# Kernel optimization log

Measured on AMD Instinct MI355X. Metric: run time of the kernel, lower is better.

Reference implementation:

```python
import jax, jax.numpy as jnp
import numpy as np

B, H, W = 1, 48, 160
CIN, CF, D = 1024, 64, 48  # input_features, PSM_features, depth_channel = max_disp/downsample
EPS = 1e-5


def setup_inputs() -> dict:
    key = jax.random.key(0)
    ks = jax.random.split(key, 12)
    z = lambda s: jnp.zeros(s, jnp.float32)
    o = lambda s: jnp.ones(s, jnp.float32)
    return {
        "left_features": jax.random.normal(ks[0], (B, CIN, H, W), jnp.float32),
        "right_features": jax.random.normal(ks[1], (B, CIN, H, W), jnp.float32),
        "conv1_w": jax.random.normal(ks[2], (CF, CIN), jnp.float32) * 0.03,
        "conv1_b": z((CF,)),
        "bn1_g": o((CF,)), "bn1_b": z((CF,)),
        "bn1_m": jax.random.normal(ks[3], (CF,), jnp.float32) * 0.1,
        "bn1_v": jax.random.uniform(ks[4], (CF,), jnp.float32) + 0.5,
        "c3a_w": jax.random.normal(ks[5], (CF, 2 * CF, 3, 3, 3), jnp.float32) * 0.02,
        "c3a_b": z((CF,)),
        "bn3a_g": o((CF,)), "bn3a_b": z((CF,)),
        "bn3a_m": jax.random.normal(ks[6], (CF,), jnp.float32) * 0.1,
        "bn3a_v": jax.random.uniform(ks[7], (CF,), jnp.float32) + 0.5,
        "c3b_w": jax.random.normal(ks[8], (CF, CF, 3, 3, 3), jnp.float32) * 0.02,
        "c3b_b": z((CF,)),
        "bn3b_g": o((CF,)), "bn3b_b": z((CF,)),
        "bn3b_m": jax.random.normal(ks[9], (CF,), jnp.float32) * 0.1,
        "bn3b_v": jax.random.uniform(ks[10], (CF,), jnp.float32) + 0.5,
    }


def _bn(x, g, b, m, v, nsp):
    # eval-mode batchnorm; nsp = number of trailing spatial dims
    sh = (-1,) + (1,) * nsp
    return (x - m.reshape(sh)) * (g.reshape(sh) * jax.lax.rsqrt(v.reshape(sh) + EPS)) + b.reshape(sh)


def reference(left_features, right_features, conv1_w, conv1_b, bn1_g, bn1_b, bn1_m, bn1_v,
              c3a_w, c3a_b, bn3a_g, bn3a_b, bn3a_m, bn3a_v,
              c3b_w, c3b_b, bn3b_g, bn3b_b, bn3b_m, bn3b_v):
    def down(x):
        y = jnp.einsum('oi,bihw->bohw', conv1_w, x) + conv1_b[:, None, None]
        return jax.nn.relu(_bn(y, bn1_g, bn1_b, bn1_m, bn1_v, 2))

    L = down(left_features)   # [B,CF,H,W]
    R = down(right_features)  # [B,CF,H,W]

    # Vectorized shifted cost volume (replaces the Python loop over disparities).
    # For disparity d, output width j: left -> L[...,j] if j>=d else 0; right -> R[...,j-d] if j>=d else 0.
    idx = jnp.arange(W)[None, :] - jnp.arange(D)[:, None]       # [D,W]
    mask = (idx >= 0).astype(L.dtype)                           # [D,W]
    left_vol = L[:, :, :, None, :] * mask                       # [B,CF,H,D,W]
    right_vol = R[:, :, :, jnp.clip(idx, 0, W - 1)] * mask      # [B,CF,H,D,W]
    cost = jnp.concatenate([left_vol, right_vol], axis=1)       # [B,2CF,H,D,W]
    cost = jnp.transpose(cost, (0, 1, 3, 2, 4))                 # [B,2CF,D,H,W]

    def conv3(x, wk, bias):
        y = jax.lax.conv_general_dilated(x, wk, (1, 1, 1), [(1, 1)] * 3,
                                         dimension_numbers=('NCDHW', 'OIDHW', 'NCDHW'))
        return y + bias[:, None, None, None]

    y = jax.nn.relu(_bn(conv3(cost, c3a_w, c3a_b), bn3a_g, bn3a_b, bn3a_m, bn3a_v, 3))
    y = jax.nn.relu(_bn(conv3(y, c3b_w, c3b_b), bn3b_g, bn3b_b, bn3b_m, bn3b_v, 3))
    return y.reshape(B, -1, H, W)  # [B, CF*D, H, W]
```

## Files before the change

kernel.cpp:

```cpp
#include <hip/hip_runtime.h>
#include <hip/hip_bf16.h>


#define HH   48
#define WW   160
#define DDEP 48
#define CIN  1024
#define NPX  (HH*WW)
#define KSPL 8

typedef unsigned short u16;
typedef unsigned int   u32;
typedef __attribute__((ext_vector_type(8))) short bf16x8;
typedef __attribute__((ext_vector_type(4))) float f32x4;
typedef __attribute__((ext_vector_type(4))) u32   u32x4;
typedef __attribute__((ext_vector_type(2))) u32   u32x2;

__device__ __forceinline__ u16 f2bf(float f) {
    u32 u = __builtin_bit_cast(u32, f);
    u32 r = u + 0x7FFFu + ((u >> 16) & 1u);
    return (u16)(r >> 16);
}

__global__ __launch_bounds__(256) void k_prep(
    const float* __restrict__ c3a, const float* __restrict__ c3b,
    const float* __restrict__ cb3a, const float* __restrict__ g3a,
    const float* __restrict__ b3a,  const float* __restrict__ m3a,
    const float* __restrict__ v3a,
    const float* __restrict__ cb3b, const float* __restrict__ g3b,
    const float* __restrict__ b3b,  const float* __restrict__ m3b,
    const float* __restrict__ v3b,
    u16* __restrict__ wa, u16* __restrict__ wb, float* __restrict__ bnc)
{
    int tid = blockIdx.x*256 + threadIdx.x;
    if (tid < 221184) {
        int i = tid & 127, o = (tid >> 7) & 63, tap = tid >> 13;
        wa[tid] = f2bf(c3a[(o*128 + i)*27 + tap]);
    } else {
        int t2 = tid - 221184;
        if (t2 < 110592) {
            int i = t2 & 63;
            int kw = (t2 >> 6) % 3;
            int rest = t2 / 192;
            int o = rest & 63, kdkh = rest >> 6;
            wb[t2] = f2bf(c3b[(o*64 + i)*27 + (kdkh/3)*9 + (kdkh%3)*3 + kw]);
        }
    }
    if (tid < 64) {
        float s = g3a[tid] * rsqrtf(v3a[tid] + 1e-5f);
        bnc[tid]      = s;
        bnc[64 + tid] = (cb3a[tid] - m3a[tid])*s + b3a[tid];
    } else if (tid < 128) {
        int o = tid - 64;
        float s = g3b[o] * rsqrtf(v3b[o] + 1e-5f);
        bnc[128 + o] = s;
        bnc[192 + o] = (cb3b[o] - m3b[o])*s + b3b[o];
    }
}

__global__ __launch_bounds__(256) void k_conv1(
    const float* __restrict__ left, const float* __restrict__ right,
    const float* __restrict__ w1, float* __restrict__ P)
{
    const int img = blockIdx.y;
    const int s   = blockIdx.z;
    const float* x = img ? right : left;
    const int px = blockIdx.x*64 + (threadIdx.x & 63);
    const int o0 = (threadIdx.x >> 6)*16;

    float acc[16];
    #pragma unroll
    for (int oo = 0; oo < 16; ++oo) acc[oo] = 0.f;

    const int ibase = s*(CIN/KSPL);
    for (int it = 0; it < CIN/KSPL; it += 4) {
        const int i = ibase + it;
        float x0 = x[(i+0)*NPX + px];
        float x1 = x[(i+1)*NPX + px];
        float x2 = x[(i+2)*NPX + px];
        float x3 = x[(i+3)*NPX + px];
        #pragma unroll
        for (int oo = 0; oo < 16; ++oo) {
            const float4 wv4 = *(const float4*)(w1 + (size_t)(o0+oo)*CIN + i);
            acc[oo] = fmaf(wv4.w, x3, fmaf(wv4.z, x2,
                      fmaf(wv4.y, x1, fmaf(wv4.x, x0, acc[oo]))));
        }
    }
    float* dst = P + ((size_t)(s*2 + img)*NPX + px)*64 + o0;
    #pragma unroll
    for (int q = 0; q < 4; ++q)
        *(f32x4*)(dst + q*4) = *(const f32x4*)(acc + q*4);
}

__global__ __launch_bounds__(256) void k_conv1_reduce(
    const float* __restrict__ P,
    const float* __restrict__ b1,
    const float* __restrict__ g,  const float* __restrict__ bb,
    const float* __restrict__ m,  const float* __restrict__ v,
    u16* __restrict__ LRb)
{
    const int tid = blockIdx.x*256 + threadIdx.x;
    const int f = tid*4;
    f32x4 acc = *(const f32x4*)(P + f);
    #pragma unroll
    for (int s = 1; s < KSPL; ++s)
        acc += *(const f32x4*)(P + (size_t)(s*2)*(NPX*64) + f);
    const int o0 = f & 63;
    u16 res[4];
    #pragma unroll
    for (int r = 0; r < 4; ++r) {
        int o = o0 + r;
        float sc = g[o] * rsqrtf(v[o] + 1e-5f);
        float val = (acc[r] + b1[o] - m[o])*sc + bb[o];
        res[r] = f2bf(val > 0.f ? val : 0.f);
    }
    *(u32x2*)(LRb + f) = *(const u32x2*)res;
}

__global__ __launch_bounds__(256) void k_conv3a(
    const u16* __restrict__ LRb, const u16* __restrict__ wa,
    const float* __restrict__ bnc, u16* __restrict__ yt)
{
    __shared__ u16 sm[31744];
    u16* Lt = sm;
    u16* Rt = sm + 11520;
    u16* Aw = sm + 23040;

    const int h  = blockIdx.x;
    const int d0 = blockIdx.y*2;
    const int tid = threadIdx.x;
    const int l  = tid & 63;
    const int wv = tid >> 6;
    const int dd = wv >> 1;
    const int wbase = (wv & 1)*80;
    const int l15 = l & 15, l4 = l >> 4;
    const int wcol = wbase + l15;
    const bf16x8 bzero = {0,0,0,0,0,0,0,0};

    f32x4 acc[4][5];
    #pragma unroll
    for (int a = 0; a < 4; ++a)
        #pragma unroll
        for (int b = 0; b < 5; ++b)
            acc[a][b] = (f32x4){0.f,0.f,0.f,0.f};

    for (int kh = 0; kh < 3; ++kh) {
        int hp = h + kh - 1;
        if (hp < 0 || hp >= HH) continue;
        __syncthreads();
        {
            const u16* ls = LRb + (size_t)hp*WW*64;
            const u16* rs = LRb + (size_t)NPX*64 + (size_t)hp*WW*64;
            #pragma unroll
            for (int gq = 0; gq < 5; ++gq) {
                int eb = (gq*256 + tid)*8;
                int wwi = eb >> 6, ii = eb & 63;
                u32x4 va = *(const u32x4*)(ls + eb);
                u32x4 vb = *(const u32x4*)(rs + eb);
                *(u32x4*)(Lt + wwi*72 + ii) = va;
                *(u32x4*)(Rt + wwi*72 + ii) = vb;
            }
        }
        for (int kd = 0; kd < 3; ++kd) {
            int dp = d0 + dd + kd - 1;
            bool dok = (dp >= 0) && (dp < DDEP);
            for (int kw = 0; kw < 3; ++kw) {
                __syncthreads();
                {
                    const u16* as = wa + (size_t)(kd*9 + kh*3 + kw)*8192;
                    #pragma unroll
                    for (int gq = 0; gq < 4; ++gq) {
                        int eb = (gq*256 + tid)*8;
                        int o = eb >> 7, ii = eb & 127;
                        *(u32x4*)(Aw + o*136 + ii) = *(const u32x4*)(as + eb);
                    }
                }
                __syncthreads();

                int laddr[5], raddr[5];
                bool val[5];
                #pragma unroll
                for (int nf = 0; nf < 5; ++nf) {
                    int wp = wcol + nf*16 + kw - 1;
                    bool vv = dok && (wp >= 0) && (wp < WW) && (wp >= dp);
                    val[nf]   = vv;
                    laddr[nf] = (vv ? wp : 0)*72;
                    raddr[nf] = (vv ? (wp - dp) : 0)*72;
                }
                #pragma unroll
                for (int ic = 0; ic < 4; ++ic) {
                    const int kcolA = ic*32 + 8*l4;
                    bf16x8 a0 = *(const bf16x8*)(Aw + ( 0 + l15)*136 + kcolA);
                    bf16x8 a1 = *(const bf16x8*)(Aw + (16 + l15)*136 + kcolA);
                    bf16x8 a2 = *(const bf16x8*)(Aw + (32 + l15)*136 + kcolA);
                    bf16x8 a3 = *(const bf16x8*)(Aw + (48 + l15)*136 + kcolA);
                    const int kin = (ic & 1)*32 + 8*l4;
                    #pragma unroll
                    for (int nf = 0; nf < 5; ++nf) {
                        const u16* bp = (ic < 2) ? (Lt + laddr[nf] + kin)
                                                 : (Rt + raddr[nf] + kin);
                        bf16x8 b = *(const bf16x8*)bp;
                        b = val[nf] ? b : bzero;
                        acc[0][nf] = __builtin_amdgcn_mfma_f32_16x16x32_bf16(a0, b, acc[0][nf], 0, 0, 0);
                        acc[1][nf] = __builtin_amdgcn_mfma_f32_16x16x32_bf16(a1, b, acc[1][nf], 0, 0, 0);
                        acc[2][nf] = __builtin_amdgcn_mfma_f32_16x16x32_bf16(a2, b, acc[2][nf], 0, 0, 0);
                        acc[3][nf] = __builtin_amdgcn_mfma_f32_16x16x32_bf16(a3, b, acc[3][nf], 0, 0, 0);
                    }
                }
            }
        }
    }

    __syncthreads();
    u16* eps = sm + wv*5280;
    float sc[4][4], sh[4][4];
    #pragma unroll
    for (int mf = 0; mf < 4; ++mf)
        #pragma unroll
        for (int r = 0; r < 4; ++r) {
            int o = mf*16 + 4*l4 + r;
            sc[mf][r] = bnc[o];
            sh[mf][r] = bnc[64 + o];
        }
    #pragma unroll
    for (int mf = 0; mf < 4; ++mf)
        #pragma unroll
        for (int nf = 0; nf < 5; ++nf)
            #pragma unroll
            for (int r = 0; r < 4; ++r) {
                float vv = acc[mf][nf][r]*sc[mf][r] + sh[mf][r];
                vv = vv > 0.f ? vv : 0.f;
                eps[(nf*16 + l15)*66 + mf*16 + 4*l4 + r] = f2bf(vv);
            }
    const size_t rowbase = (size_t)((d0 + dd)*HH + h)*WW + wbase;
    u16* yb = yt + rowbase*64;
    #pragma unroll
    for (int k = 0; k < 40; ++k) {
        int flat = k*64 + l;
        int n = flat >> 5, odw = (flat & 31)*2;
        u32 vv = *(const u32*)(eps + n*66 + odw);
        *(u32*)(yb + (size_t)n*64 + odw) = vv;
    }
}

__global__ __launch_bounds__(256) void k_conv3b(
    const u16* __restrict__ yt, const u16* __restrict__ wb,
    const float* __restrict__ bnc, float* __restrict__ outp)
{
    __shared__ u16 sm2[35840];
    u16* Bt0 = sm2;
    u16* Bt1 = sm2 + 11520;
    u16* A2  = sm2 + 23040;

    const int h  = blockIdx.x;
    const int d0 = blockIdx.y*2;
    const int tid = threadIdx.x;
    const int l  = tid & 63;
    const int wv = tid >> 6;
    const int dd = wv >> 1;
    const int wbase = (wv & 1)*80;
    const int l15 = l & 15, l4 = l >> 4;
    const int wcol = wbase + l15;
    const bf16x8 bzero = {0,0,0,0,0,0,0,0};

    f32x4 acc[4][5];
    #pragma unroll
    for (int a = 0; a < 4; ++a)
        #pragma unroll
        for (int b = 0; b < 5; ++b)
            acc[a][b] = (f32x4){0.f,0.f,0.f,0.f};

    for (int kh = 0; kh < 3; ++kh) {
        int hp = h + kh - 1;
        if (hp < 0 || hp >= HH) continue;
        for (int kd = 0; kd < 3; ++kd) {
            __syncthreads();
            {
                int dpa = d0 + kd - 1, dpb = d0 + kd;
                int ca = min(max(dpa, 0), DDEP-1);
                int cb = min(max(dpb, 0), DDEP-1);
                const u16* s0 = yt + ((size_t)(ca*HH + hp)*WW)*64;
                const u16* s1 = yt + ((size_t)(cb*HH + hp)*WW)*64;
                #pragma unroll
                for (int gq = 0; gq < 5; ++gq) {
                    int eb = (gq*256 + tid)*8;
                    int wwi = eb >> 6, ii = eb & 63;
                    *(u32x4*)(Bt0 + wwi*72 + ii) = *(const u32x4*)(s0 + eb);
                    *(u32x4*)(Bt1 + wwi*72 + ii) = *(const u32x4*)(s1 + eb);
                }
                const u16* as = wb + (size_t)(kd*3 + kh)*12288;
                #pragma unroll
                for (int gq = 0; gq < 6; ++gq) {
                    int idx = gq*256 + tid;
                    int o = idx/24;
                    int c = (idx - o*24)*8;
                    *(u32x4*)(A2 + o*200 + c) = *(const u32x4*)(as + (size_t)idx*8);
                }
            }
            __syncthreads();

            int dpw = d0 + dd + kd - 1;
            bool dok = (dpw >= 0) && (dpw < DDEP);
            const u16* Bt = dd ? Bt1 : Bt0;
            for (int kw = 0; kw < 3; ++kw) {
                int baddr[5]; bool val[5];
                #pragma unroll
                for (int nf = 0; nf < 5; ++nf) {
                    int wp = wcol + nf*16 + kw - 1;
                    bool vv = dok && (wp >= 0) && (wp < WW);
                    val[nf]   = vv;
                    baddr[nf] = (vv ? wp : 0)*72;
                }
                #pragma unroll
                for (int ic = 0; ic < 2; ++ic) {
                    const int kcolA = kw*64 + ic*32 + 8*l4;
                    bf16x8 a0 = *(const bf16x8*)(A2 + ( 0 + l15)*200 + kcolA);
                    bf16x8 a1 = *(const bf16x8*)(A2 + (16 + l15)*200 + kcolA);
                    bf16x8 a2 = *(const bf16x8*)(A2 + (32 + l15)*200 + kcolA);
                    bf16x8 a3 = *(const bf16x8*)(A2 + (48 + l15)*200 + kcolA);
                    const int kin = ic*32 + 8*l4;
                    #pragma unroll
                    for (int nf = 0; nf < 5; ++nf) {
                        bf16x8 b = *(const bf16x8*)(Bt + baddr[nf] + kin);
                        b = val[nf] ? b : bzero;
                        acc[0][nf] = __builtin_amdgcn_mfma_f32_16x16x32_bf16(a0, b, acc[0][nf], 0, 0, 0);
                        acc[1][nf] = __builtin_amdgcn_mfma_f32_16x16x32_bf16(a1, b, acc[1][nf], 0, 0, 0);
                        acc[2][nf] = __builtin_amdgcn_mfma_f32_16x16x32_bf16(a2, b, acc[2][nf], 0, 0, 0);
                        acc[3][nf] = __builtin_amdgcn_mfma_f32_16x16x32_bf16(a3, b, acc[3][nf], 0, 0, 0);
                    }
                }
            }
        }
    }

    const int dout = d0 + dd;
    #pragma unroll
    for (int mf = 0; mf < 4; ++mf)
        #pragma unroll
        for (int r = 0; r < 4; ++r) {
            int o = mf*16 + 4*l4 + r;
            float s = bnc[128 + o], t = bnc[192 + o];
            size_t base = ((size_t)(o*DDEP + dout)*HH + h)*WW + wbase;
            #pragma unroll
            for (int nf = 0; nf < 5; ++nf) {
                float vv = acc[mf][nf][r]*s + t;
                outp[base + nf*16 + l15] = vv > 0.f ? vv : 0.f;
            }
        }
}

extern "C" void kernel_launch(void* const* d_in, const int* in_sizes, int n_in,
                              void* d_out, int out_size, void* d_ws, size_t ws_size,
                              hipStream_t stream)
{
    const float* left  = (const float*)d_in[0];
    const float* right = (const float*)d_in[1];
    const float* w1    = (const float*)d_in[2];
    const float* b1    = (const float*)d_in[3];
    const float* g1    = (const float*)d_in[4];
    const float* bb1   = (const float*)d_in[5];
    const float* m1    = (const float*)d_in[6];
    const float* v1    = (const float*)d_in[7];
    const float* c3a   = (const float*)d_in[8];
    const float* cb3a  = (const float*)d_in[9];
    const float* g3a   = (const float*)d_in[10];
    const float* b3a   = (const float*)d_in[11];
    const float* m3a   = (const float*)d_in[12];
    const float* v3a   = (const float*)d_in[13];
    const float* c3b   = (const float*)d_in[14];
    const float* cb3b  = (const float*)d_in[15];
    const float* g3b   = (const float*)d_in[16];
    const float* b3b   = (const float*)d_in[17];
    const float* m3b   = (const float*)d_in[18];
    const float* v3b   = (const float*)d_in[19];

    char* ws = (char*)d_ws;
    u16*   LRb = (u16*)ws;
    u16*   wa  = (u16*)(ws + 1966080);
    u16*   wb  = (u16*)(ws + 1966080 + 442368);
    float* bnc = (float*)(ws + 1966080 + 442368 + 221184);
    u16*   yt  = (u16*)(ws + 1966080 + 442368 + 221184 + 1024);
    if (ws_size < 49816576) return;

    float* P = (float*)d_out;

    k_prep<<<dim3(1296), dim3(256), 0, stream>>>(
        c3a, c3b, cb3a, g3a, b3a, m3a, v3a, cb3b, g3b, b3b, m3b, v3b, wa, wb, bnc);
    k_conv1<<<dim3(120, 2, KSPL), dim3(256), 0, stream>>>(
        left, right, w1, P);
    k_conv1_reduce<<<dim3(960), dim3(256), 0, stream>>>(
        P, b1, g1, bb1, m1, v1, LRb);
    k_conv3a<<<dim3(48, 24), dim3(256), 0, stream>>>(LRb, wa, bnc, yt);
    k_conv3b<<<dim3(48, 24), dim3(256), 0, stream>>>(yt, wb, bnc, (float*)d_out);
}
```

Baseline: 384.4 us.

## Double-buffer conv3a weight tiles and flatten tap loop to cut barriers

Flattens the kh/kd/kw loops in the first 3D conv into one tap loop and double-buffers the per-tap weight tile in shared memory. The next tap's weights load while the current tap's MFMAs run, so most taps need one barrier instead of two. This adds about 17 KB of LDS per block, which may lower occupancy. The prefetch is a synchronous load-then-store, so the overlap comes mostly from removing the barrier.

```diff
diff --git a/kernel.cpp b/kernel.cpp
--- a/kernel.cpp
+++ b/kernel.cpp
@@ -121,10 +121,11 @@
     const u16* __restrict__ LRb, const u16* __restrict__ wa,
     const float* __restrict__ bnc, u16* __restrict__ yt)
 {
-    __shared__ u16 sm[31744];
-    u16* Lt = sm;
-    u16* Rt = sm + 11520;
-    u16* Aw = sm + 23040;
+    __shared__ u16 sm[40448];
+    u16* Lt  = sm;
+    u16* Rt  = sm + 11520;
+    u16* Aw0 = sm + 23040;
+    u16* Aw1 = sm + 31744;
 
     const int h  = blockIdx.x;
     const int d0 = blockIdx.y*2;
@@ -144,13 +145,27 @@
         for (int b = 0; b < 5; ++b)
             acc[a][b] = (f32x4){0.f,0.f,0.f,0.f};
 
-    for (int kh = 0; kh < 3; ++kh) {
-        int hp = h + kh - 1;
-        if (hp < 0 || hp >= HH) continue;
+    const int kh_lo = (h == 0) ? 1 : 0;
+    const int kh_hi = (h == HH-1) ? 1 : 2;
+    const int ntap = (kh_hi - kh_lo + 1)*9;
+
+    {
+        const u16* as = wa + (size_t)(kh_lo*3)*8192;
+        #pragma unroll
+        for (int gq = 0; gq < 4; ++gq) {
+            int eb = (gq*256 + tid)*8;
+            *(u32x4*)(Aw0 + (eb>>7)*136 + (eb&127)) = *(const u32x4*)(as + eb);
+        }
+    }
+
+    int kh = kh_lo, kd = 0, kw = 0, buf = 0;
+    for (int i = 0; i < ntap; ++i) {
         __syncthreads();
-        {
+        const bool newrow = (kd == 0 && kw == 0);
+        if (newrow) {
+            const int hp = h + kh - 1;
             const u16* ls = LRb + (size_t)hp*WW*64;
-            const u16* rs = LRb + (size_t)NPX*64 + (size_t)hp*WW*64;
+            const u16* rs = LRb + (size_t)(NPX + hp*WW)*64;
             #pragma unroll
             for (int gq = 0; gq < 5; ++gq) {
                 int eb = (gq*256 + tid)*8;
@@ -161,54 +176,53 @@
                 *(u32x4*)(Rt + wwi*72 + ii) = vb;
             }
         }
-        for (int kd = 0; kd < 3; ++kd) {
-            int dp = d0 + dd + kd - 1;
-            bool dok = (dp >= 0) && (dp < DDEP);
-            for (int kw = 0; kw < 3; ++kw) {
-                __syncthreads();
-                {
-                    const u16* as = wa + (size_t)(kd*9 + kh*3 + kw)*8192;
-                    #pragma unroll
-                    for (int gq = 0; gq < 4; ++gq) {
-                        int eb = (gq*256 + tid)*8;
-                        int o = eb >> 7, ii = eb & 127;
-                        *(u32x4*)(Aw + o*136 + ii) = *(const u32x4*)(as + eb);
-                    }
-                }
-                __syncthreads();
-
-                int laddr[5], raddr[5];
-                bool val[5];
-                #pragma unroll
-                for (int nf = 0; nf < 5; ++nf) {
-                    int wp = wcol + nf*16 + kw - 1;
-                    bool vv = dok && (wp >= 0) && (wp < WW) && (wp >= dp);
-                    val[nf]   = vv;
-                    laddr[nf] = (vv ? wp : 0)*72;
-                    raddr[nf] = (vv ? (wp - dp) : 0)*72;
-                }
-                #pragma unroll
-                for (int ic = 0; ic < 4; ++ic) {
-                    const int kcolA = ic*32 + 8*l4;
-                    bf16x8 a0 = *(const bf16x8*)(Aw + ( 0 + l15)*136 + kcolA);
-                    bf16x8 a1 = *(const bf16x8*)(Aw + (16 + l15)*136 + kcolA);
-                    bf16x8 a2 = *(const bf16x8*)(Aw + (32 + l15)*136 + kcolA);
-                    bf16x8 a3 = *(const bf16x8*)(Aw + (48 + l15)*136 + kcolA);
-                    const int kin = (ic & 1)*32 + 8*l4;
-                    #pragma unroll
-                    for (int nf = 0; nf < 5; ++nf) {
-                        const u16* bp = (ic < 2) ? (Lt + laddr[nf] + kin)
-                                                 : (Rt + raddr[nf] + kin);
-                        bf16x8 b = *(const bf16x8*)bp;
-                        b = val[nf] ? b : bzero;
-                        acc[0][nf] = __builtin_amdgcn_mfma_f32_16x16x32_bf16(a0, b, acc[0][nf], 0, 0, 0);
-                        acc[1][nf] = __builtin_amdgcn_mfma_f32_16x16x32_bf16(a1, b, acc[1][nf], 0, 0, 0);
-                        acc[2][nf] = __builtin_amdgcn_mfma_f32_16x16x32_bf16(a2, b, acc[2][nf], 0, 0, 0);
-                        acc[3][nf] = __builtin_amdgcn_mfma_f32_16x16x32_bf16(a3, b, acc[3][nf], 0, 0, 0);
-                    }
-                }
-            }
-        }
+        int nkw = kw + 1, nkd = kd, nkh = kh;
+        if (nkw == 3) { nkw = 0; ++nkd; if (nkd == 3) { nkd = 0; ++nkh; } }
+        if (i + 1 < ntap) {
+            const u16* as = wa + (size_t)(nkd*9 + nkh*3 + nkw)*8192;
+            u16* awn = buf ? Aw0 : Aw1;
+            #pragma unroll
+            for (int gq = 0; gq < 4; ++gq) {
+                int eb = (gq*256 + tid)*8;
+                *(u32x4*)(awn + (eb>>7)*136 + (eb&127)) = *(const u32x4*)(as + eb);
+            }
+        }
+        if (newrow) __syncthreads();
+
+        const u16* Awc = buf ? Aw1 : Aw0;
+        const int dp = d0 + dd + kd - 1;
+        const bool dok = (dp >= 0) && (dp < DDEP);
+        int laddr[5], raddr[5];
+        bool val[5];
+        #pragma unroll
+        for (int nf = 0; nf < 5; ++nf) {
+            int wp = wcol + nf*16 + kw - 1;
+            bool vv = dok && (wp >= 0) && (wp < WW) && (wp >= dp);
+            val[nf]   = vv;
+            laddr[nf] = (vv ? wp : 0)*72;
+            raddr[nf] = (vv ? (wp - dp) : 0)*72;
+        }
+        #pragma unroll
+        for (int ic = 0; ic < 4; ++ic) {
+            const int kcolA = ic*32 + 8*l4;
+            bf16x8 a0 = *(const bf16x8*)(Awc + ( 0 + l15)*136 + kcolA);
+            bf16x8 a1 = *(const bf16x8*)(Awc + (16 + l15)*136 + kcolA);
+            bf16x8 a2 = *(const bf16x8*)(Awc + (32 + l15)*136 + kcolA);
+            bf16x8 a3 = *(const bf16x8*)(Awc + (48 + l15)*136 + kcolA);
+            const int kin = (ic & 1)*32 + 8*l4;
+            #pragma unroll
+            for (int nf = 0; nf < 5; ++nf) {
+                const u16* bp = (ic < 2) ? (Lt + laddr[nf] + kin)
+                                         : (Rt + raddr[nf] + kin);
+                bf16x8 b = *(const bf16x8*)bp;
+                b = val[nf] ? b : bzero;
+                acc[0][nf] = __builtin_amdgcn_mfma_f32_16x16x32_bf16(a0, b, acc[0][nf], 0, 0, 0);
+                acc[1][nf] = __builtin_amdgcn_mfma_f32_16x16x32_bf16(a1, b, acc[1][nf], 0, 0, 0);
+                acc[2][nf] = __builtin_amdgcn_mfma_f32_16x16x32_bf16(a2, b, acc[2][nf], 0, 0, 0);
+                acc[3][nf] = __builtin_amdgcn_mfma_f32_16x16x32_bf16(a3, b, acc[3][nf], 0, 0, 0);
+            }
+        }
+        buf ^= 1; kw = nkw; kd = nkd; kh = nkh;
     }
 
     __syncthreads();
```

After: 389.6 us. No clear change (+1.3%).

## Store conv3a output channel-blocked and read conv3b B operand directly from global

Applied to the files above, without the earlier changes.

The intermediate activation is now written in a channel-blocked layout (8-channel groups, each a contiguous row of W×8 values), so each lane's bf16x8 B fragment is a single contiguous 16-byte global load. The conv3b kernel stops staging the activation rows in LDS and loads B fragments straight from global/L2. Only the weights stay in shared memory. This removes LDS traffic and shrinks LDS use, which may raise occupancy, but global load latency now sits directly in the MFMA inner loop.

```diff
diff --git a/kernel.cpp b/kernel.cpp
--- a/kernel.cpp
+++ b/kernel.cpp
@@ -150,7 +150,7 @@
         __syncthreads();
         {
             const u16* ls = LRb + (size_t)hp*WW*64;
-            const u16* rs = LRb + (size_t)NPX*64 + (size_t)hp*WW*64;
+            const u16* rs = LRb + (size_t)(NPX + hp*WW)*64;
             #pragma unroll
             for (int gq = 0; gq < 5; ++gq) {
                 int eb = (gq*256 + tid)*8;
@@ -232,14 +232,17 @@
                 vv = vv > 0.f ? vv : 0.f;
                 eps[(nf*16 + l15)*66 + mf*16 + 4*l4 + r] = f2bf(vv);
             }
-    const size_t rowbase = (size_t)((d0 + dd)*HH + h)*WW + wbase;
-    u16* yb = yt + rowbase*64;
+    const int dy = d0 + dd;
+    u16* yb2 = yt + ((size_t)(dy*HH + h)*8)*1280;
     #pragma unroll
     for (int k = 0; k < 40; ++k) {
         int flat = k*64 + l;
-        int n = flat >> 5, odw = (flat & 31)*2;
-        u32 vv = *(const u32*)(eps + n*66 + odw);
-        *(u32*)(yb + (size_t)n*64 + odw) = vv;
+        int c   = flat / 320;
+        int rem = flat - c*320;
+        int w   = rem >> 2;
+        int pr  = (rem & 3)*2;
+        u32 vv = *(const u32*)(eps + w*66 + c*8 + pr);
+        *(u32*)(yb2 + (size_t)c*1280 + (wbase + w)*8 + pr) = vv;
     }
 }
 
@@ -247,10 +250,7 @@
     const u16* __restrict__ yt, const u16* __restrict__ wb,
     const float* __restrict__ bnc, float* __restrict__ outp)
 {
-    __shared__ u16 sm2[35840];
-    u16* Bt0 = sm2;
-    u16* Bt1 = sm2 + 11520;
-    u16* A2  = sm2 + 23040;
+    __shared__ u16 A2[12800];
 
     const int h  = blockIdx.x;
     const int d0 = blockIdx.y*2;
@@ -276,40 +276,29 @@
         for (int kd = 0; kd < 3; ++kd) {
             __syncthreads();
             {
-                int dpa = d0 + kd - 1, dpb = d0 + kd;
-                int ca = min(max(dpa, 0), DDEP-1);
-                int cb = min(max(dpb, 0), DDEP-1);
-                const u16* s0 = yt + ((size_t)(ca*HH + hp)*WW)*64;
-                const u16* s1 = yt + ((size_t)(cb*HH + hp)*WW)*64;
-                #pragma unroll
-                for (int gq = 0; gq < 5; ++gq) {
-                    int eb = (gq*256 + tid)*8;
-                    int wwi = eb >> 6, ii = eb & 63;
-                    *(u32x4*)(Bt0 + wwi*72 + ii) = *(const u32x4*)(s0 + eb);
-                    *(u32x4*)(Bt1 + wwi*72 + ii) = *(const u32x4*)(s1 + eb);
-                }
                 const u16* as = wb + (size_t)(kd*3 + kh)*12288;
                 #pragma unroll
-                for (int gq = 0; gq < 6; ++gq) {
-                    int idx = gq*256 + tid;
+                for (int q = 0; q < 6; ++q) {
+                    int idx = q*256 + tid;
                     int o = idx/24;
-                    int c = (idx - o*24)*8;
-                    *(u32x4*)(A2 + o*200 + c) = *(const u32x4*)(as + (size_t)idx*8);
+                    int cc = (idx - o*24)*8;
+                    *(u32x4*)(A2 + o*200 + cc) = *(const u32x4*)(as + (size_t)idx*8);
                 }
             }
             __syncthreads();
 
-            int dpw = d0 + dd + kd - 1;
-            bool dok = (dpw >= 0) && (dpw < DDEP);
-            const u16* Bt = dd ? Bt1 : Bt0;
+            const int dpw = d0 + dd + kd - 1;
+            const bool dok = (dpw >= 0) && (dpw < DDEP);
+            const int dc = min(max(dpw, 0), DDEP-1);
+            const u16* yrow = yt + ((size_t)((dc*HH + hp)*8) + l4)*1280;
             for (int kw = 0; kw < 3; ++kw) {
-                int baddr[5]; bool val[5];
+                int gofs[5]; bool val[5];
                 #pragma unroll
                 for (int nf = 0; nf < 5; ++nf) {
                     int wp = wcol + nf*16 + kw - 1;
                     bool vv = dok && (wp >= 0) && (wp < WW);
-                    val[nf]   = vv;
-                    baddr[nf] = (vv ? wp : 0)*72;
+                    val[nf]  = vv;
+                    gofs[nf] = (vv ? wp : 0)*8;
                 }
                 #pragma unroll
                 for (int ic = 0; ic < 2; ++ic) {
@@ -318,10 +307,10 @@
                     bf16x8 a1 = *(const bf16x8*)(A2 + (16 + l15)*200 + kcolA);
                     bf16x8 a2 = *(const bf16x8*)(A2 + (32 + l15)*200 + kcolA);
                     bf16x8 a3 = *(const bf16x8*)(A2 + (48 + l15)*200 + kcolA);
-                    const int kin = ic*32 + 8*l4;
+                    const u16* yc = yrow + ic*5120;
                     #pragma unroll
                     for (int nf = 0; nf < 5; ++nf) {
-                        bf16x8 b = *(const bf16x8*)(Bt + baddr[nf] + kin);
+                        bf16x8 b = *(const bf16x8*)(yc + gofs[nf]);
                         b = val[nf] ? b : bzero;
                         acc[0][nf] = __builtin_amdgcn_mfma_f32_16x16x32_bf16(a0, b, acc[0][nf], 0, 0, 0);
                         acc[1][nf] = __builtin_amdgcn_mfma_f32_16x16x32_bf16(a1, b, acc[1][nf], 0, 0, 0);
```

After: 389.7 us. No clear change (+1.4%).
